# Kernel optimization log

Hardware: AMD Instinct MI355X
Metric: run time of the kernel (lower is better)

The kernel has to match this reference:

```python
import jax, jax.numpy as jnp
import numpy as np

B, G, A, C = 128, 16, 8732, 21
THR = 0.5        # overlap_threshold
NEG_POS = 3      # neg_pos_ratio
VAR0, VAR1 = 0.1, 0.2  # loc_variance


def center_to_point(b):
    cxcy, wh = b[:, :2], b[:, 2:]
    return jnp.concatenate([cxcy - wh / 2, cxcy + wh / 2], axis=-1)


def iou_matrix(a, b):
    # a: [G,4], b: [A,4] point coords (x1,y1,x2,y2) -> [G,A]
    tl = jnp.maximum(a[:, None, :2], b[None, :, :2])
    br = jnp.minimum(a[:, None, 2:], b[None, :, 2:])
    wh = jnp.clip(br - tl, 0.0)
    inter = wh[..., 0] * wh[..., 1]
    area_a = (a[:, 2] - a[:, 0]) * (a[:, 3] - a[:, 1])
    area_b = (b[:, 2] - b[:, 0]) * (b[:, 3] - b[:, 1])
    return inter / (area_a[:, None] + area_b[None, :] - inter)


def encode(anchors, gt_pt):
    # anchors [A,4] (cx,cy,w,h); gt_pt [A,4] point coords
    g_cxcy = (gt_pt[:, :2] + gt_pt[:, 2:]) / 2
    g_wh = gt_pt[:, 2:] - gt_pt[:, :2]
    d_cxcy = (g_cxcy - anchors[:, :2]) / (anchors[:, 2:] * VAR0)
    d_wh = jnp.log(g_wh / anchors[:, 2:]) / VAR1
    return jnp.concatenate([d_cxcy, d_wh], axis=-1)


def match(boxes, labels, anchors, anchors_pt):
    # boxes [G,4] point coords, labels [G] int
    iou = iou_matrix(boxes, anchors_pt)           # [G,A]
    anchor_index = jnp.argmax(iou, axis=1)        # best anchor per gt, [G]
    gt_overlap = jnp.max(iou, axis=0)             # best gt overlap per anchor, [A]
    gt_index = jnp.argmax(iou, axis=0)            # best gt per anchor, [A]
    gt_overlap = gt_overlap.at[anchor_index].set(1.0)
    for i in range(G):
        gt_index = gt_index.at[anchor_index[i]].set(i)
    gt_coords = boxes[gt_index]                   # [A,4]
    loc = encode(anchors, gt_coords)              # [A,4]
    conf = labels[gt_index] + 1                   # [A], 0 reserved for background
    conf = jnp.where(gt_overlap < THR, 0, conf)
    return loc, conf


def setup_inputs() -> dict:
    key = jax.random.key(0)
    k1, k2, k3, k4, k5, k6, k7 = jax.random.split(key, 7)
    predict_offset_coords = jax.random.normal(k1, (B, A, 4), jnp.float32)
    predict_confidences = jax.random.normal(k2, (B, A, C), jnp.float32)
    # valid gt boxes: centers in [0.2,0.8], sizes in [0.05,0.3]
    c = jax.random.uniform(k3, (B, G, 2)) * 0.6 + 0.2
    s = jax.random.uniform(k4, (B, G, 2)) * 0.25 + 0.05
    target_boxes = jnp.concatenate([c - s / 2, c + s / 2], axis=-1)
    target_labels = jax.random.randint(k5, (B, G), 0, C - 1).astype(jnp.int32)
    # anchors in center-coord form (cx,cy,w,h), strictly positive w,h
    acx = jax.random.uniform(k6, (A, 2)) * 0.9 + 0.05
    awh = jax.random.uniform(k7, (A, 2)) * 0.25 + 0.05
    anchors = jnp.concatenate([acx, awh], axis=-1)
    return {"predict_offset_coords": predict_offset_coords,
            "predict_confidences": predict_confidences,
            "target_boxes": target_boxes,
            "target_labels": target_labels,
            "anchors": anchors}


def reference(predict_offset_coords, predict_confidences, target_boxes, target_labels, anchors):
    anchors_pt = center_to_point(anchors)
    loc_t, conf_t = jax.vmap(match, in_axes=(0, 0, None, None))(
        target_boxes, target_labels, anchors, anchors_pt)
    # labels are built without grad in the original (fresh tensors)
    loc_t = jax.lax.stop_gradient(loc_t)
    conf_t = jax.lax.stop_gradient(conf_t)

    is_pos = conf_t > 0                            # [B,A]
    # smooth L1 (beta=1), summed over positive anchors
    diff = predict_offset_coords - loc_t
    ad = jnp.abs(diff)
    sl1 = jnp.where(ad < 1.0, 0.5 * diff * diff, ad - 0.5)
    loss_loc = jnp.sum(sl1 * is_pos[..., None])

    num_pos = jnp.sum(is_pos, axis=1, keepdims=True)      # [B,1]
    n_total = jnp.sum(num_pos).astype(jnp.float32)
    num_neg = jnp.minimum(NEG_POS * num_pos, A - 1)        # [B,1]

    logp = jax.nn.log_softmax(predict_confidences, axis=-1)
    nll = -jnp.take_along_axis(logp, conf_t[..., None], axis=-1)[..., 0]  # [B,A]

    # hard-negative mining via double argsort
    aux = jnp.where(is_pos, 0.0, nll)
    order = jnp.argsort(-aux, axis=1)
    rank = jnp.argsort(order, axis=1)
    is_neg = rank < num_neg

    sel = jnp.logical_or(is_pos, is_neg)
    loss_cls = jnp.sum(jnp.where(sel, nll, 0.0))
    return loss_loc / n_total, loss_cls / n_total
```

## Files before the change

kernel.cpp:

```cpp
#include <hip/hip_runtime.h>
#include <math.h>

#define B_ 128
#define G_ 16
#define A_ 8732
#define C_ 21
#define THR_ 0.5f
#define NEG_POS_ 3
#define VAR0_ 0.1f
#define VAR1_ 0.2f

#define BA_   (B_ * A_)
#define NTH_  (BA_ / 4)
#define NBLK_ ((NTH_ + 255) / 256)

struct Accum { float loss_loc; float loss_cls; int n_total; int pad; };

__global__ void k_init(Accum* acc) {
    acc->loss_loc = 0.f;
    acc->loss_cls = 0.f;
    acc->n_total  = 0;
}

__global__ __launch_bounds__(512) void k_match(
    const float* __restrict__ tboxes,
    const int*   __restrict__ tlabels,
    const float* __restrict__ anchors,
    int*         __restrict__ match,
    int*         __restrict__ num_pos,
    Accum*                    acc)
{
    const int b    = blockIdx.x;
    const int tid  = threadIdx.x;
    const int lane = tid & 63;
    const int w    = tid >> 6;

    __shared__ float         s_ov[A_];
    __shared__ unsigned char s_gi[A_];
    __shared__ float s_boxlds[G_ * 4];
    __shared__ int   s_lab[G_];
    __shared__ unsigned long long s_gb[8 * G_];
    __shared__ int   s_forced[G_];
    __shared__ int   s_cnt[8];

    if (tid < G_ * 4) s_boxlds[tid] = tboxes[b * G_ * 4 + tid];
    if (tid < G_)     s_lab[tid]    = tlabels[b * G_ + tid];
    __syncthreads();

    float bx0[G_], by0[G_], bx1[G_], by1[G_], bar[G_];
    #pragma unroll
    for (int g = 0; g < G_; ++g) {
        bx0[g] = s_boxlds[g * 4 + 0];
        by0[g] = s_boxlds[g * 4 + 1];
        bx1[g] = s_boxlds[g * 4 + 2];
        by1[g] = s_boxlds[g * 4 + 3];
        bar[g] = (bx1[g] - bx0[g]) * (by1[g] - by0[g]);
    }

    unsigned long long gb[G_];
    #pragma unroll
    for (int g = 0; g < G_; ++g) gb[g] = 0ull;

    for (int a = tid; a < A_; a += 512) {
        float4 an = ((const float4*)anchors)[a];
        float ax0 = an.x - an.z * 0.5f, ay0 = an.y - an.w * 0.5f;
        float ax1 = an.x + an.z * 0.5f, ay1 = an.y + an.w * 0.5f;
        float area_b = (ax1 - ax0) * (ay1 - ay0);
        float bov = -1.f; int bg = 0;
        #pragma unroll
        for (int g = 0; g < G_; ++g) {
            float tlx = fmaxf(bx0[g], ax0);
            float tly = fmaxf(by0[g], ay0);
            float brx = fminf(bx1[g], ax1);
            float bry = fminf(by1[g], ay1);
            float wdt = fmaxf(brx - tlx, 0.f);
            float hgt = fmaxf(bry - tly, 0.f);
            float inter = wdt * hgt;
            float iou = inter / (bar[g] + area_b - inter);
            if (iou > bov) { bov = iou; bg = g; }
            unsigned long long pk =
                ((unsigned long long)__float_as_uint(iou) << 32) |
                (unsigned)(~(unsigned)a);
            if (pk > gb[g]) gb[g] = pk;
        }
        s_ov[a] = bov;
        s_gi[a] = (unsigned char)bg;
    }

    #pragma unroll
    for (int g = 0; g < G_; ++g) {
        #pragma unroll
        for (int off = 32; off > 0; off >>= 1) {
            unsigned long long o = __shfl_down(gb[g], off);
            if (o > gb[g]) gb[g] = o;
        }
    }
    if (lane == 0) {
        #pragma unroll
        for (int g = 0; g < G_; ++g) s_gb[w * G_ + g] = gb[g];
    }
    __syncthreads();
    if (tid < G_) {
        unsigned long long m = 0ull;
        #pragma unroll
        for (int wv = 0; wv < 8; ++wv) {
            unsigned long long v = s_gb[wv * G_ + tid];
            if (v > m) m = v;
        }
        s_forced[tid] = (int)(~(unsigned)(m & 0xFFFFFFFFull));
    }
    __syncthreads();
    if (tid == 0) {
        for (int g = 0; g < G_; ++g) {
            int a = s_forced[g];
            s_ov[a] = 1.0f;
            s_gi[a] = (unsigned char)g;
        }
    }
    __syncthreads();

    int cnt = 0;
    for (int a = tid; a < A_; a += 512) {
        float ov = s_ov[a];
        int g = s_gi[a];
        int conf = (ov < THR_) ? 0 : (s_lab[g] + 1);
        match[b * A_ + a] = conf | (g << 8);
        cnt += (conf > 0);
    }
    #pragma unroll
    for (int off = 32; off > 0; off >>= 1) cnt += __shfl_down(cnt, off);
    if (lane == 0) s_cnt[w] = cnt;
    __syncthreads();
    if (tid == 0) {
        int t = 0;
        #pragma unroll
        for (int wv = 0; wv < 8; ++wv) t += s_cnt[wv];
        num_pos[b] = t;
        atomicAdd(&acc->n_total, t);
    }
}

__global__ __launch_bounds__(256) void k_loss(
    const float* __restrict__ pred_off,
    const float* __restrict__ pred_conf,
    const float* __restrict__ tboxes,
    const float* __restrict__ anchors,
    const int*   __restrict__ match,
    float*       __restrict__ aux,
    float*       __restrict__ part_loc,
    float*       __restrict__ part_cls)
{
    const int tid  = threadIdx.x;
    const int t    = blockIdx.x * 256 + tid;
    const int lane = tid & 63;
    const int w    = tid >> 6;

    __shared__ float s_lloc[4];
    __shared__ float s_pnll[4];

    float lloc = 0.f, pnll = 0.f;

    if (t < NTH_) {
        const float4* cp = (const float4*)pred_conf + (size_t)t * 21;
        float xx[84];
        #pragma unroll
        for (int k = 0; k < 21; ++k) {
            float4 v = cp[k];
            xx[4 * k + 0] = v.x; xx[4 * k + 1] = v.y;
            xx[4 * k + 2] = v.z; xx[4 * k + 3] = v.w;
        }
        int4 mk = ((const int4*)match)[t];
        int mkv[4]; mkv[0] = mk.x; mkv[1] = mk.y; mkv[2] = mk.z; mkv[3] = mk.w;
        float auxv[4];

        #pragma unroll
        for (int j = 0; j < 4; ++j) {
            const int base = 21 * j;
            float m = xx[base];
            #pragma unroll
            for (int c = 1; c < C_; ++c) m = fmaxf(m, xx[base + c]);
            float s = 0.f;
            #pragma unroll
            for (int c = 0; c < C_; ++c) s += __expf(xx[base + c] - m);
            float lse = m + __logf(s);

            int conf = mkv[j] & 0xff;
            int g    = mkv[j] >> 8;
            float xc = xx[base];
            #pragma unroll
            for (int c = 1; c < C_; ++c) xc = (conf == c) ? xx[base + c] : xc;
            float nll = lse - xc;
            bool pos = conf > 0;
            auxv[j] = pos ? 0.f : nll;

            if (pos) {
                pnll += nll;
                int i = t * 4 + j;
                int b = i / A_;
                int a = i - b * A_;
                float4 an = ((const float4*)anchors)[a];
                float4 bx = ((const float4*)tboxes)[b * G_ + g];
                float gcx = (bx.x + bx.z) * 0.5f, gcy = (bx.y + bx.w) * 0.5f;
                float gw = bx.z - bx.x, gh = bx.w - bx.y;
                float l0 = (gcx - an.x) / (an.z * VAR0_);
                float l1 = (gcy - an.y) / (an.w * VAR0_);
                float l2 = logf(gw / an.z) / VAR1_;
                float l3 = logf(gh / an.w) / VAR1_;
                float4 p = ((const float4*)pred_off)[i];
                float d, ad;
                d = p.x - l0; ad = fabsf(d); lloc += (ad < 1.f) ? 0.5f * d * d : ad - 0.5f;
                d = p.y - l1; ad = fabsf(d); lloc += (ad < 1.f) ? 0.5f * d * d : ad - 0.5f;
                d = p.z - l2; ad = fabsf(d); lloc += (ad < 1.f) ? 0.5f * d * d : ad - 0.5f;
                d = p.w - l3; ad = fabsf(d); lloc += (ad < 1.f) ? 0.5f * d * d : ad - 0.5f;
            }
        }
        ((float4*)aux)[t] = make_float4(auxv[0], auxv[1], auxv[2], auxv[3]);
    }

    #pragma unroll
    for (int off = 32; off > 0; off >>= 1) {
        lloc += __shfl_down(lloc, off);
        pnll += __shfl_down(pnll, off);
    }
    if (lane == 0) { s_lloc[w] = lloc; s_pnll[w] = pnll; }
    __syncthreads();
    if (tid == 0) {
        part_loc[blockIdx.x] = s_lloc[0] + s_lloc[1] + s_lloc[2] + s_lloc[3];
        part_cls[blockIdx.x] = s_pnll[0] + s_pnll[1] + s_pnll[2] + s_pnll[3];
    }
}

#define NPT_ 35
__global__ __launch_bounds__(256) void k_select(
    const float* __restrict__ aux,
    const int*   __restrict__ num_pos,
    Accum*                    acc)
{
    const int b    = blockIdx.x;
    const int tid  = threadIdx.x;
    const int lane = tid & 63;
    const int w    = tid >> 6;

    __shared__ int   s_c[2][4];
    __shared__ int   s_cf[4];
    __shared__ float s_sf[4];

    unsigned u[NPT_];
    #pragma unroll
    for (int j = 0; j < NPT_; ++j) {
        int a = tid + j * 256;
        u[j] = (a < A_) ? __float_as_uint(aux[(size_t)b * A_ + a]) : 0u;
    }

    const int K = min(NEG_POS_ * num_pos[b], A_ - 1);

    unsigned lo = 0u, hi = 0x7f800000u;
    int it = 0;
    while (lo < hi) {
        unsigned mid = (lo + hi) >> 1;
        int c = 0;
        #pragma unroll
        for (int j = 0; j < NPT_; ++j) c += (u[j] > mid);
        #pragma unroll
        for (int off = 32; off > 0; off >>= 1) c += __shfl_down(c, off);
        if (lane == 0) s_c[it & 1][w] = c;
        __syncthreads();
        int total = s_c[it & 1][0] + s_c[it & 1][1] + s_c[it & 1][2] + s_c[it & 1][3];
        if (total >= K) lo = mid + 1; else hi = mid;
        ++it;
    }

    int c = 0; float sm = 0.f;
    #pragma unroll
    for (int j = 0; j < NPT_; ++j) {
        if (u[j] > lo) { c++; sm += __uint_as_float(u[j]); }
    }
    #pragma unroll
    for (int off = 32; off > 0; off >>= 1) {
        c  += __shfl_down(c, off);
        sm += __shfl_down(sm, off);
    }
    if (lane == 0) { s_cf[w] = c; s_sf[w] = sm; }
    __syncthreads();
    if (tid == 0) {
        int   ct = s_cf[0] + s_cf[1] + s_cf[2] + s_cf[3];
        float st = s_sf[0] + s_sf[1] + s_sf[2] + s_sf[3];
        float T = __uint_as_float(lo);
        atomicAdd(&acc->loss_cls, st + (float)(K - ct) * T);
    }
}

__global__ __launch_bounds__(256) void k_final(
    const Accum* __restrict__ acc,
    const float* __restrict__ part_loc,
    const float* __restrict__ part_cls,
    float*       __restrict__ out)
{
    const int tid  = threadIdx.x;
    const int lane = tid & 63;
    const int w    = tid >> 6;
    __shared__ float s_l[4], s_cl[4];

    float L = 0.f, Cc = 0.f;
    for (int i = tid; i < NBLK_; i += 256) { L += part_loc[i]; Cc += part_cls[i]; }
    #pragma unroll
    for (int off = 32; off > 0; off >>= 1) {
        L  += __shfl_down(L, off);
        Cc += __shfl_down(Cc, off);
    }
    if (lane == 0) { s_l[w] = L; s_cl[w] = Cc; }
    __syncthreads();
    if (tid == 0) {
        float n = (float)acc->n_total;
        float lloc = s_l[0] + s_l[1] + s_l[2] + s_l[3];
        float lcls = s_cl[0] + s_cl[1] + s_cl[2] + s_cl[3] + acc->loss_cls;
        out[0] = lloc / n;
        out[1] = lcls / n;
    }
}

extern "C" void kernel_launch(void* const* d_in, const int* in_sizes, int n_in,
                              void* d_out, int out_size, void* d_ws, size_t ws_size,
                              hipStream_t stream) {
    const float* pred_off  = (const float*)d_in[0];
    const float* pred_conf = (const float*)d_in[1];
    const float* tboxes    = (const float*)d_in[2];
    const int*   tlabels   = (const int*)  d_in[3];
    const float* anchors   = (const float*)d_in[4];
    float* out = (float*)d_out;

    char* ws = (char*)d_ws;
    int*   match_ws = (int*)ws;     ws += (size_t)BA_ * sizeof(int);
    float* aux_ws   = (float*)ws;   ws += (size_t)BA_ * sizeof(float);
    float* ploc_ws  = (float*)ws;   ws += (size_t)((NBLK_ + 3) & ~3) * sizeof(float);
    float* pcls_ws  = (float*)ws;   ws += (size_t)((NBLK_ + 3) & ~3) * sizeof(float);
    int*   npos_ws  = (int*)ws;     ws += (size_t)((B_ + 3) & ~3) * sizeof(int);
    Accum* acc      = (Accum*)ws;

    k_init<<<1, 1, 0, stream>>>(acc);
    k_match<<<B_, 512, 0, stream>>>(tboxes, tlabels, anchors, match_ws, npos_ws, acc);
    k_loss<<<NBLK_, 256, 0, stream>>>(pred_off, pred_conf, tboxes, anchors,
                                      match_ws, aux_ws, ploc_ws, pcls_ws);
    k_select<<<B_, 256, 0, stream>>>(aux_ws, npos_ws, acc);
    k_final<<<1, 256, 0, stream>>>(acc, ploc_ws, pcls_ws, out);
}
```

Baseline: 232.5 us.

## Fuse match, loss and hard-negative selection into one per-batch kernel

```diff
diff --git a/kernel.cpp b/kernel.cpp
--- a/kernel.cpp
+++ b/kernel.cpp
@@ -10,25 +10,20 @@
 #define VAR0_ 0.1f
 #define VAR1_ 0.2f
 
-#define BA_   (B_ * A_)
-#define NTH_  (BA_ / 4)
-#define NBLK_ ((NTH_ + 255) / 256)
-
-struct Accum { float loss_loc; float loss_cls; int n_total; int pad; };
-
-__global__ void k_init(Accum* acc) {
-    acc->loss_loc = 0.f;
-    acc->loss_cls = 0.f;
-    acc->n_total  = 0;
-}
-
-__global__ __launch_bounds__(512) void k_match(
+#define TPB_  768
+#define NW_   (TPB_ / 64)
+#define NGRP_ (A_ / 4)
+#define NPTS_ 12
+
+__global__ __launch_bounds__(TPB_) void k_fused(
+    const float* __restrict__ pred_off,
+    const float* __restrict__ pred_conf,
     const float* __restrict__ tboxes,
     const int*   __restrict__ tlabels,
     const float* __restrict__ anchors,
-    int*         __restrict__ match,
-    int*         __restrict__ num_pos,
-    Accum*                    acc)
+    float*       __restrict__ part_loc,
+    float*       __restrict__ part_cls,
+    int*         __restrict__ num_pos)
 {
     const int b    = blockIdx.x;
     const int tid  = threadIdx.x;
@@ -39,9 +34,12 @@
     __shared__ unsigned char s_gi[A_];
     __shared__ float s_boxlds[G_ * 4];
     __shared__ int   s_lab[G_];
-    __shared__ unsigned long long s_gb[8 * G_];
+    __shared__ unsigned long long s_gb[NW_ * G_];
     __shared__ int   s_forced[G_];
-    __shared__ int   s_cnt[8];
+    __shared__ int   s_i1[NW_];
+    __shared__ float s_f1[NW_], s_f2[NW_], s_f3[NW_];
+    __shared__ int   s_c[2][NW_];
+    __shared__ int   s_K;
 
     if (tid < G_ * 4) s_boxlds[tid] = tboxes[b * G_ * 4 + tid];
     if (tid < G_)     s_lab[tid]    = tlabels[b * G_ + tid];
@@ -61,7 +59,7 @@
     #pragma unroll
     for (int g = 0; g < G_; ++g) gb[g] = 0ull;
 
-    for (int a = tid; a < A_; a += 512) {
+    for (int a = tid; a < A_; a += TPB_) {
         float4 an = ((const float4*)anchors)[a];
         float ax0 = an.x - an.z * 0.5f, ay0 = an.y - an.w * 0.5f;
         float ax1 = an.x + an.z * 0.5f, ay1 = an.y + an.w * 0.5f;
@@ -103,7 +101,7 @@
     if (tid < G_) {
         unsigned long long m = 0ull;
         #pragma unroll
-        for (int wv = 0; wv < 8; ++wv) {
+        for (int wv = 0; wv < NW_; ++wv) {
             unsigned long long v = s_gb[wv * G_ + tid];
             if (v > m) m = v;
         }
@@ -119,140 +117,79 @@
     }
     __syncthreads();
 
-    int cnt = 0;
-    for (int a = tid; a < A_; a += 512) {
-        float ov = s_ov[a];
-        int g = s_gi[a];
-        int conf = (ov < THR_) ? 0 : (s_lab[g] + 1);
-        match[b * A_ + a] = conf | (g << 8);
-        cnt += (conf > 0);
-    }
-    #pragma unroll
-    for (int off = 32; off > 0; off >>= 1) cnt += __shfl_down(cnt, off);
-    if (lane == 0) s_cnt[w] = cnt;
-    __syncthreads();
-    if (tid == 0) {
-        int t = 0;
-        #pragma unroll
-        for (int wv = 0; wv < 8; ++wv) t += s_cnt[wv];
-        num_pos[b] = t;
-        atomicAdd(&acc->n_total, t);
-    }
-}
-
-__global__ __launch_bounds__(256) void k_loss(
-    const float* __restrict__ pred_off,
-    const float* __restrict__ pred_conf,
-    const float* __restrict__ tboxes,
-    const float* __restrict__ anchors,
-    const int*   __restrict__ match,
-    float*       __restrict__ aux,
-    float*       __restrict__ part_loc,
-    float*       __restrict__ part_cls)
-{
-    const int tid  = threadIdx.x;
-    const int t    = blockIdx.x * 256 + tid;
-    const int lane = tid & 63;
-    const int w    = tid >> 6;
-
-    __shared__ float s_lloc[4];
-    __shared__ float s_pnll[4];
-
     float lloc = 0.f, pnll = 0.f;
-
-    if (t < NTH_) {
-        const float4* cp = (const float4*)pred_conf + (size_t)t * 21;
-        float xx[84];
-        #pragma unroll
-        for (int k = 0; k < 21; ++k) {
-            float4 v = cp[k];
-            xx[4 * k + 0] = v.x; xx[4 * k + 1] = v.y;
-            xx[4 * k + 2] = v.z; xx[4 * k + 3] = v.w;
-        }
-        int4 mk = ((const int4*)match)[t];
-        int mkv[4]; mkv[0] = mk.x; mkv[1] = mk.y; mkv[2] = mk.z; mkv[3] = mk.w;
-        float auxv[4];
-
-        #pragma unroll
-        for (int j = 0; j < 4; ++j) {
-            const int base = 21 * j;
-            float m = xx[base];
+    int   cnt  = 0;
+
+    for (int j = 0; j < 3; ++j) {
+        int gid = tid + j * TPB_;
+        if (gid < NGRP_) {
+            const float4* cp = (const float4*)pred_conf + ((size_t)b * NGRP_ + gid) * 21;
+            float xx[84];
             #pragma unroll
-            for (int c = 1; c < C_; ++c) m = fmaxf(m, xx[base + c]);
-            float s = 0.f;
+            for (int k = 0; k < 21; ++k) {
+                float4 v = cp[k];
+                xx[4 * k + 0] = v.x; xx[4 * k + 1] = v.y;
+                xx[4 * k + 2] = v.z; xx[4 * k + 3] = v.w;
+            }
             #pragma unroll
-            for (int c = 0; c < C_; ++c) s += __expf(xx[base + c] - m);
-            float lse = m + __logf(s);
-
-            int conf = mkv[j] & 0xff;
-            int g    = mkv[j] >> 8;
-            float xc = xx[base];
-            #pragma unroll
-            for (int c = 1; c < C_; ++c) xc = (conf == c) ? xx[base + c] : xc;
-            float nll = lse - xc;
-            bool pos = conf > 0;
-            auxv[j] = pos ? 0.f : nll;
-
-            if (pos) {
-                pnll += nll;
-                int i = t * 4 + j;
-                int b = i / A_;
-                int a = i - b * A_;
-                float4 an = ((const float4*)anchors)[a];
-                float4 bx = ((const float4*)tboxes)[b * G_ + g];
-                float gcx = (bx.x + bx.z) * 0.5f, gcy = (bx.y + bx.w) * 0.5f;
-                float gw = bx.z - bx.x, gh = bx.w - bx.y;
-                float l0 = (gcx - an.x) / (an.z * VAR0_);
-                float l1 = (gcy - an.y) / (an.w * VAR0_);
-                float l2 = logf(gw / an.z) / VAR1_;
-                float l3 = logf(gh / an.w) / VAR1_;
-                float4 p = ((const float4*)pred_off)[i];
-                float d, ad;
-                d = p.x - l0; ad = fabsf(d); lloc += (ad < 1.f) ? 0.5f * d * d : ad - 0.5f;
-                d = p.y - l1; ad = fabsf(d); lloc += (ad < 1.f) ? 0.5f * d * d : ad - 0.5f;
-                d = p.z - l2; ad = fabsf(d); lloc += (ad < 1.f) ? 0.5f * d * d : ad - 0.5f;
-                d = p.w - l3; ad = fabsf(d); lloc += (ad < 1.f) ? 0.5f * d * d : ad - 0.5f;
+            for (int jj = 0; jj < 4; ++jj) {
+                const int base = 21 * jj;
+                const int a    = 4 * gid + jj;
+                float ov = s_ov[a];
+                int   g  = s_gi[a];
+                int conf = (ov < THR_) ? 0 : (s_lab[g] + 1);
+
+                float m = xx[base];
+                #pragma unroll
+                for (int c = 1; c < C_; ++c) m = fmaxf(m, xx[base + c]);
+                float s = 0.f;
+                #pragma unroll
+                for (int c = 0; c < C_; ++c) s += __expf(xx[base + c] - m);
+                float lse = m + __logf(s);
+
+                float xc = xx[base];
+                #pragma unroll
+                for (int c = 1; c < C_; ++c) xc = (conf == c) ? xx[base + c] : xc;
+                float nll = lse - xc;
+                bool pos = conf > 0;
+                s_ov[a] = pos ? 0.f : nll;
+
+                if (pos) {
+                    cnt++;
+                    pnll += nll;
+                    float4 an = ((const float4*)anchors)[a];
+                    float4 bx = ((const float4*)tboxes)[b * G_ + g];
+                    float gcx = (bx.x + bx.z) * 0.5f, gcy = (bx.y + bx.w) * 0.5f;
+                    float gw = bx.z - bx.x, gh = bx.w - bx.y;
+                    float l0 = (gcx - an.x) / (an.z * VAR0_);
+                    float l1 = (gcy - an.y) / (an.w * VAR0_);
+                    float l2 = logf(gw / an.z) / VAR1_;
+                    float l3 = logf(gh / an.w) / VAR1_;
+                    float4 p = ((const float4*)pred_off)[(size_t)b * A_ + a];
+                    float d, ad;
+                    d = p.x - l0; ad = fabsf(d); lloc += (ad < 1.f) ? 0.5f * d * d : ad - 0.5f;
+                    d = p.y - l1; ad = fabsf(d); lloc += (ad < 1.f) ? 0.5f * d * d : ad - 0.5f;
+                    d = p.z - l2; ad = fabsf(d); lloc += (ad < 1.f) ? 0.5f * d * d : ad - 0.5f;
+                    d = p.w - l3; ad = fabsf(d); lloc += (ad < 1.f) ? 0.5f * d * d : ad - 0.5f;
+                }
             }
         }
-        ((float4*)aux)[t] = make_float4(auxv[0], auxv[1], auxv[2], auxv[3]);
-    }
-
-    #pragma unroll
-    for (int off = 32; off > 0; off >>= 1) {
-        lloc += __shfl_down(lloc, off);
-        pnll += __shfl_down(pnll, off);
-    }
-    if (lane == 0) { s_lloc[w] = lloc; s_pnll[w] = pnll; }
-    __syncthreads();
-    if (tid == 0) {
-        part_loc[blockIdx.x] = s_lloc[0] + s_lloc[1] + s_lloc[2] + s_lloc[3];
-        part_cls[blockIdx.x] = s_pnll[0] + s_pnll[1] + s_pnll[2] + s_pnll[3];
-    }
-}
-
-#define NPT_ 35
-__global__ __launch_bounds__(256) void k_select(
-    const float* __restrict__ aux,
-    const int*   __restrict__ num_pos,
-    Accum*                    acc)
-{
-    const int b    = blockIdx.x;
-    const int tid  = threadIdx.x;
-    const int lane = tid & 63;
-    const int w    = tid >> 6;
-
-    __shared__ int   s_c[2][4];
-    __shared__ int   s_cf[4];
-    __shared__ float s_sf[4];
-
-    unsigned u[NPT_];
-    #pragma unroll
-    for (int j = 0; j < NPT_; ++j) {
-        int a = tid + j * 256;
-        u[j] = (a < A_) ? __float_as_uint(aux[(size_t)b * A_ + a]) : 0u;
-    }
-
-    const int K = min(NEG_POS_ * num_pos[b], A_ - 1);
+    }
+
+    int cw = cnt;
+    #pragma unroll
+    for (int off = 32; off > 0; off >>= 1) cw += __shfl_down(cw, off);
+    if (lane == 0) s_i1[w] = cw;
+    __syncthreads();
+    if (tid == 0) {
+        int np = 0;
+        #pragma unroll
+        for (int wv = 0; wv < NW_; ++wv) np += s_i1[wv];
+        num_pos[b] = np;
+        s_K = min(NEG_POS_ * np, A_ - 1);
+    }
+    __syncthreads();
+    const int K = s_K;
 
     unsigned lo = 0u, hi = 0x7f800000u;
     int it = 0;
@@ -260,62 +197,78 @@
         unsigned mid = (lo + hi) >> 1;
         int c = 0;
         #pragma unroll
-        for (int j = 0; j < NPT_; ++j) c += (u[j] > mid);
+        for (int j = 0; j < NPTS_; ++j) {
+            int a = tid + j * TPB_;
+            if (a < A_) c += (__float_as_uint(s_ov[a]) > mid);
+        }
         #pragma unroll
         for (int off = 32; off > 0; off >>= 1) c += __shfl_down(c, off);
         if (lane == 0) s_c[it & 1][w] = c;
         __syncthreads();
-        int total = s_c[it & 1][0] + s_c[it & 1][1] + s_c[it & 1][2] + s_c[it & 1][3];
+        int total = 0;
+        #pragma unroll
+        for (int wv = 0; wv < NW_; ++wv) total += s_c[it & 1][wv];
         if (total >= K) lo = mid + 1; else hi = mid;
         ++it;
     }
 
-    int c = 0; float sm = 0.f;
-    #pragma unroll
-    for (int j = 0; j < NPT_; ++j) {
-        if (u[j] > lo) { c++; sm += __uint_as_float(u[j]); }
-    }
+    int c2 = 0; float sm = 0.f;
+    #pragma unroll
+    for (int j = 0; j < NPTS_; ++j) {
+        int a = tid + j * TPB_;
+        if (a < A_) {
+            unsigned u = __float_as_uint(s_ov[a]);
+            if (u > lo) { c2++; sm += __uint_as_float(u); }
+        }
+    }
+
     #pragma unroll
     for (int off = 32; off > 0; off >>= 1) {
-        c  += __shfl_down(c, off);
-        sm += __shfl_down(sm, off);
-    }
-    if (lane == 0) { s_cf[w] = c; s_sf[w] = sm; }
-    __syncthreads();
-    if (tid == 0) {
-        int   ct = s_cf[0] + s_cf[1] + s_cf[2] + s_cf[3];
-        float st = s_sf[0] + s_sf[1] + s_sf[2] + s_sf[3];
+        lloc += __shfl_down(lloc, off);
+        pnll += __shfl_down(pnll, off);
+        sm   += __shfl_down(sm, off);
+        c2   += __shfl_down(c2, off);
+    }
+    if (lane == 0) { s_f1[w] = lloc; s_f2[w] = pnll; s_f3[w] = sm; s_i1[w] = c2; }
+    __syncthreads();
+    if (tid == 0) {
+        float L = 0.f, P = 0.f, S = 0.f; int Ct = 0;
+        #pragma unroll
+        for (int wv = 0; wv < NW_; ++wv) {
+            L += s_f1[wv]; P += s_f2[wv]; S += s_f3[wv]; Ct += s_i1[wv];
+        }
         float T = __uint_as_float(lo);
-        atomicAdd(&acc->loss_cls, st + (float)(K - ct) * T);
+        part_loc[b] = L;
+        part_cls[b] = P + S + (float)(K - Ct) * T;
     }
 }
 
-__global__ __launch_bounds__(256) void k_final(
-    const Accum* __restrict__ acc,
+__global__ __launch_bounds__(128) void k_final(
     const float* __restrict__ part_loc,
     const float* __restrict__ part_cls,
+    const int*   __restrict__ num_pos,
     float*       __restrict__ out)
 {
     const int tid  = threadIdx.x;
     const int lane = tid & 63;
     const int w    = tid >> 6;
-    __shared__ float s_l[4], s_cl[4];
-
-    float L = 0.f, Cc = 0.f;
-    for (int i = tid; i < NBLK_; i += 256) { L += part_loc[i]; Cc += part_cls[i]; }
+    __shared__ float s_l[2], s_c[2];
+    __shared__ int   s_n[2];
+
+    float L = part_loc[tid], Cc = part_cls[tid];
+    int   N = num_pos[tid];
     #pragma unroll
     for (int off = 32; off > 0; off >>= 1) {
         L  += __shfl_down(L, off);
         Cc += __shfl_down(Cc, off);
-    }
-    if (lane == 0) { s_l[w] = L; s_cl[w] = Cc; }
-    __syncthreads();
-    if (tid == 0) {
-        float n = (float)acc->n_total;
-        float lloc = s_l[0] + s_l[1] + s_l[2] + s_l[3];
-        float lcls = s_cl[0] + s_cl[1] + s_cl[2] + s_cl[3] + acc->loss_cls;
-        out[0] = lloc / n;
-        out[1] = lcls / n;
+        N  += __shfl_down(N, off);
+    }
+    if (lane == 0) { s_l[w] = L; s_c[w] = Cc; s_n[w] = N; }
+    __syncthreads();
+    if (tid == 0) {
+        float n = (float)(s_n[0] + s_n[1]);
+        out[0] = (s_l[0] + s_l[1]) / n;
+        out[1] = (s_c[0] + s_c[1]) / n;
     }
 }
 
@@ -330,17 +283,11 @@
     float* out = (float*)d_out;
 
     char* ws = (char*)d_ws;
-    int*   match_ws = (int*)ws;     ws += (size_t)BA_ * sizeof(int);
-    float* aux_ws   = (float*)ws;   ws += (size_t)BA_ * sizeof(float);
-    float* ploc_ws  = (float*)ws;   ws += (size_t)((NBLK_ + 3) & ~3) * sizeof(float);
-    float* pcls_ws  = (float*)ws;   ws += (size_t)((NBLK_ + 3) & ~3) * sizeof(float);
-    int*   npos_ws  = (int*)ws;     ws += (size_t)((B_ + 3) & ~3) * sizeof(int);
-    Accum* acc      = (Accum*)ws;
-
-    k_init<<<1, 1, 0, stream>>>(acc);
-    k_match<<<B_, 512, 0, stream>>>(tboxes, tlabels, anchors, match_ws, npos_ws, acc);
-    k_loss<<<NBLK_, 256, 0, stream>>>(pred_off, pred_conf, tboxes, anchors,
-                                      match_ws, aux_ws, ploc_ws, pcls_ws);
-    k_select<<<B_, 256, 0, stream>>>(aux_ws, npos_ws, acc);
-    k_final<<<1, 256, 0, stream>>>(acc, ploc_ws, pcls_ws, out);
+    float* ploc_ws = (float*)ws;   ws += (size_t)B_ * sizeof(float);
+    float* pcls_ws = (float*)ws;   ws += (size_t)B_ * sizeof(float);
+    int*   npos_ws = (int*)ws;     ws += (size_t)B_ * sizeof(int);
+
+    k_fused<<<B_, TPB_, 0, stream>>>(pred_off, pred_conf, tboxes, tlabels, anchors,
+                                     ploc_ws, pcls_ws, npos_ws);
+    k_final<<<1, 128, 0, stream>>>(ploc_ws, pcls_ws, npos_ws, out);
 }
```

New measurement: 234.9 us. About the same (+1.1%).

## Fold init and final kernels into neighbors, use atomics and last-block finalize

Applied to the files above, without the earlier changes.

```diff
diff --git a/kernel.cpp b/kernel.cpp
--- a/kernel.cpp
+++ b/kernel.cpp
@@ -14,15 +14,12 @@
 #define NTH_  (BA_ / 4)
 #define NBLK_ ((NTH_ + 255) / 256)
 
-struct Accum { float loss_loc; float loss_cls; int n_total; int pad; };
-
-__global__ void k_init(Accum* acc) {
-    acc->loss_loc = 0.f;
-    acc->loss_cls = 0.f;
-    acc->n_total  = 0;
-}
-
-__global__ __launch_bounds__(512) void k_match(
+#define MTPB_ 768
+#define MNW_  (MTPB_ / 64)
+
+struct Accum { float loss_loc; float loss_cls; int done; int pad; };
+
+__global__ __launch_bounds__(MTPB_) void k_match(
     const float* __restrict__ tboxes,
     const int*   __restrict__ tlabels,
     const float* __restrict__ anchors,
@@ -35,13 +32,19 @@
     const int lane = tid & 63;
     const int w    = tid >> 6;
 
+    if (b == 0 && tid == 0) {
+        acc->loss_loc = 0.f;
+        acc->loss_cls = 0.f;
+        acc->done     = 0;
+    }
+
     __shared__ float         s_ov[A_];
     __shared__ unsigned char s_gi[A_];
     __shared__ float s_boxlds[G_ * 4];
     __shared__ int   s_lab[G_];
-    __shared__ unsigned long long s_gb[8 * G_];
+    __shared__ unsigned long long s_gb[MNW_ * G_];
     __shared__ int   s_forced[G_];
-    __shared__ int   s_cnt[8];
+    __shared__ int   s_cnt[MNW_];
 
     if (tid < G_ * 4) s_boxlds[tid] = tboxes[b * G_ * 4 + tid];
     if (tid < G_)     s_lab[tid]    = tlabels[b * G_ + tid];
@@ -61,7 +64,7 @@
     #pragma unroll
     for (int g = 0; g < G_; ++g) gb[g] = 0ull;
 
-    for (int a = tid; a < A_; a += 512) {
+    for (int a = tid; a < A_; a += MTPB_) {
         float4 an = ((const float4*)anchors)[a];
         float ax0 = an.x - an.z * 0.5f, ay0 = an.y - an.w * 0.5f;
         float ax1 = an.x + an.z * 0.5f, ay1 = an.y + an.w * 0.5f;
@@ -103,7 +106,7 @@
     if (tid < G_) {
         unsigned long long m = 0ull;
         #pragma unroll
-        for (int wv = 0; wv < 8; ++wv) {
+        for (int wv = 0; wv < MNW_; ++wv) {
             unsigned long long v = s_gb[wv * G_ + tid];
             if (v > m) m = v;
         }
@@ -120,7 +123,7 @@
     __syncthreads();
 
     int cnt = 0;
-    for (int a = tid; a < A_; a += 512) {
+    for (int a = tid; a < A_; a += MTPB_) {
         float ov = s_ov[a];
         int g = s_gi[a];
         int conf = (ov < THR_) ? 0 : (s_lab[g] + 1);
@@ -134,9 +137,8 @@
     if (tid == 0) {
         int t = 0;
         #pragma unroll
-        for (int wv = 0; wv < 8; ++wv) t += s_cnt[wv];
+        for (int wv = 0; wv < MNW_; ++wv) t += s_cnt[wv];
         num_pos[b] = t;
-        atomicAdd(&acc->n_total, t);
     }
 }
 
@@ -147,8 +149,7 @@
     const float* __restrict__ anchors,
     const int*   __restrict__ match,
     float*       __restrict__ aux,
-    float*       __restrict__ part_loc,
-    float*       __restrict__ part_cls)
+    Accum*                    acc)
 {
     const int tid  = threadIdx.x;
     const int t    = blockIdx.x * 256 + tid;
@@ -225,8 +226,10 @@
     if (lane == 0) { s_lloc[w] = lloc; s_pnll[w] = pnll; }
     __syncthreads();
     if (tid == 0) {
-        part_loc[blockIdx.x] = s_lloc[0] + s_lloc[1] + s_lloc[2] + s_lloc[3];
-        part_cls[blockIdx.x] = s_pnll[0] + s_pnll[1] + s_pnll[2] + s_pnll[3];
+        float L = s_lloc[0] + s_lloc[1] + s_lloc[2] + s_lloc[3];
+        float P = s_pnll[0] + s_pnll[1] + s_pnll[2] + s_pnll[3];
+        if (L != 0.f) atomicAdd(&acc->loss_loc, L);
+        if (P != 0.f) atomicAdd(&acc->loss_cls, P);
     }
 }
 
@@ -234,7 +237,8 @@
 __global__ __launch_bounds__(256) void k_select(
     const float* __restrict__ aux,
     const int*   __restrict__ num_pos,
-    Accum*                    acc)
+    Accum*                    acc,
+    float*       __restrict__ out)
 {
     const int b    = blockIdx.x;
     const int tid  = threadIdx.x;
@@ -244,6 +248,7 @@
     __shared__ int   s_c[2][4];
     __shared__ int   s_cf[4];
     __shared__ float s_sf[4];
+    __shared__ int   s_last;
 
     unsigned u[NPT_];
     #pragma unroll
@@ -287,35 +292,25 @@
         float st = s_sf[0] + s_sf[1] + s_sf[2] + s_sf[3];
         float T = __uint_as_float(lo);
         atomicAdd(&acc->loss_cls, st + (float)(K - ct) * T);
-    }
-}
-
-__global__ __launch_bounds__(256) void k_final(
-    const Accum* __restrict__ acc,
-    const float* __restrict__ part_loc,
-    const float* __restrict__ part_cls,
-    float*       __restrict__ out)
-{
-    const int tid  = threadIdx.x;
-    const int lane = tid & 63;
-    const int w    = tid >> 6;
-    __shared__ float s_l[4], s_cl[4];
-
-    float L = 0.f, Cc = 0.f;
-    for (int i = tid; i < NBLK_; i += 256) { L += part_loc[i]; Cc += part_cls[i]; }
-    #pragma unroll
-    for (int off = 32; off > 0; off >>= 1) {
-        L  += __shfl_down(L, off);
-        Cc += __shfl_down(Cc, off);
-    }
-    if (lane == 0) { s_l[w] = L; s_cl[w] = Cc; }
-    __syncthreads();
-    if (tid == 0) {
-        float n = (float)acc->n_total;
-        float lloc = s_l[0] + s_l[1] + s_l[2] + s_l[3];
-        float lcls = s_cl[0] + s_cl[1] + s_cl[2] + s_cl[3] + acc->loss_cls;
-        out[0] = lloc / n;
-        out[1] = lcls / n;
+        __threadfence();
+        int prev = atomicAdd(&acc->done, 1);
+        s_last = (prev == B_ - 1) ? 1 : 0;
+    }
+    __syncthreads();
+
+    if (s_last) {
+        int n = (tid < B_) ? num_pos[tid] : 0;
+        #pragma unroll
+        for (int off = 32; off > 0; off >>= 1) n += __shfl_down(n, off);
+        if (lane == 0) s_cf[w] = n;
+        __syncthreads();
+        if (tid == 0) {
+            float nt = (float)(s_cf[0] + s_cf[1]);
+            float L  = atomicAdd(&acc->loss_loc, 0.f);
+            float Cc = atomicAdd(&acc->loss_cls, 0.f);
+            out[0] = L / nt;
+            out[1] = Cc / nt;
+        }
     }
 }
 
@@ -332,15 +327,11 @@
     char* ws = (char*)d_ws;
     int*   match_ws = (int*)ws;     ws += (size_t)BA_ * sizeof(int);
     float* aux_ws   = (float*)ws;   ws += (size_t)BA_ * sizeof(float);
-    float* ploc_ws  = (float*)ws;   ws += (size_t)((NBLK_ + 3) & ~3) * sizeof(float);
-    float* pcls_ws  = (float*)ws;   ws += (size_t)((NBLK_ + 3) & ~3) * sizeof(float);
     int*   npos_ws  = (int*)ws;     ws += (size_t)((B_ + 3) & ~3) * sizeof(int);
     Accum* acc      = (Accum*)ws;
 
-    k_init<<<1, 1, 0, stream>>>(acc);
-    k_match<<<B_, 512, 0, stream>>>(tboxes, tlabels, anchors, match_ws, npos_ws, acc);
+    k_match<<<B_, MTPB_, 0, stream>>>(tboxes, tlabels, anchors, match_ws, npos_ws, acc);
     k_loss<<<NBLK_, 256, 0, stream>>>(pred_off, pred_conf, tboxes, anchors,
-                                      match_ws, aux_ws, ploc_ws, pcls_ws);
-    k_select<<<B_, 256, 0, stream>>>(aux_ws, npos_ws, acc);
-    k_final<<<1, 256, 0, stream>>>(acc, ploc_ws, pcls_ws, out);
+                                      match_ws, aux_ws, acc);
+    k_select<<<B_, 256, 0, stream>>>(aux_ws, npos_ws, acc, out);
 }
```

Result: slower. 237.3 us (+2.1%).
